# Performance work log

Hardware: AMD Instinct MI355X
Metric: run time of the kernel (lower is better)

The kernel has to match this reference:

```python
import jax, jax.numpy as jnp
import numpy as np

N_ENT = 100000
N_REL = 24
N_BASES = 8
HID = 256
N_EDGES = 1000000
N_TRIPLES = 65536


def _rgcn_layer(x, src, dst, edge_type, norm, basis, comp, root, bias):
    # x: [N, d]; basis: [B, d, d]; comp: [R, B]; root: [d, d]; bias: [d]
    x_src = x[src]                    # [E, d] gather
    coef = comp[edge_type]            # [E, B]
    out = x @ root + bias             # root/self transform
    # W_r = sum_b comp[r,b] * basis_b is linear, so aggregate coefficient- and
    # norm-weighted source features per basis, then apply basis once at node level.
    for b in range(basis.shape[0]):
        w = (coef[:, b] * norm)[:, None] * x_src          # [E, d]
        agg = jax.ops.segment_sum(w, dst, num_segments=N_ENT)  # [N, d]
        out = out + agg @ basis[b]
    return out


def _edge_norm(dst, edge_type):
    # PyG RGCNConv propagates per relation with aggr='mean': normalize by
    # in-degree of dst counted within each relation type.
    key = dst * N_REL + edge_type
    cnt = jax.ops.segment_sum(jnp.ones_like(key, dtype=jnp.float32), key,
                              num_segments=N_ENT * N_REL)
    return 1.0 / jnp.maximum(cnt[key], 1.0)


def setup_inputs() -> dict:
    key = jax.random.key(0)
    ks = jax.random.split(key, 16)
    d = HID
    xav_e = float(np.sqrt(6.0 / (N_ENT + d)))
    xav_r = float(np.sqrt(6.0 / (N_REL + d)))
    xav_w = float(np.sqrt(6.0 / (d + d)))
    inp = {
        'entity_emb': jax.random.uniform(ks[0], (N_ENT, d), jnp.float32, -xav_e, xav_e),
        'rel_emb': jax.random.uniform(ks[1], (N_REL, d), jnp.float32, -xav_r, xav_r),
        'basis1': jax.random.uniform(ks[2], (N_BASES, d, d), jnp.float32, -xav_w, xav_w),
        'comp1': jax.random.normal(ks[3], (N_REL, N_BASES), jnp.float32) / np.sqrt(N_BASES),
        'root1': jax.random.uniform(ks[4], (d, d), jnp.float32, -xav_w, xav_w),
        'bias1': jnp.zeros((d,), jnp.float32),
        'basis2': jax.random.uniform(ks[5], (N_BASES, d, d), jnp.float32, -xav_w, xav_w),
        'comp2': jax.random.normal(ks[6], (N_REL, N_BASES), jnp.float32) / np.sqrt(N_BASES),
        'root2': jax.random.uniform(ks[7], (d, d), jnp.float32, -xav_w, xav_w),
        'bias2': jnp.zeros((d,), jnp.float32),
        'edge_index': jax.random.randint(ks[8], (2, N_EDGES), 0, N_ENT, jnp.int32),
        'edge_type': jax.random.randint(ks[9], (N_EDGES,), 0, N_REL, jnp.int32),
        'heads': jax.random.randint(ks[10], (N_TRIPLES,), 0, N_ENT, jnp.int32),
        'rels': jax.random.randint(ks[11], (N_TRIPLES,), 0, N_REL, jnp.int32),
        'tails': jax.random.randint(ks[12], (N_TRIPLES,), 0, N_ENT, jnp.int32),
    }
    return inp


def reference(entity_emb, rel_emb, basis1, comp1, root1, bias1,
              basis2, comp2, root2, bias2,
              edge_index, edge_type, heads, rels, tails):
    src, dst = edge_index[0], edge_index[1]
    norm = _edge_norm(dst, edge_type)
    # eval mode: no edge dropout, feature dropout is identity
    x = entity_emb
    x = jax.nn.relu(_rgcn_layer(x, src, dst, edge_type, norm, basis1, comp1, root1, bias1))
    x = jax.nn.relu(_rgcn_layer(x, src, dst, edge_type, norm, basis2, comp2, root2, bias2))
    # DistMult score: sum(h * r * t)
    scores = jnp.sum(x[heads] * rel_emb[rels] * x[tails], axis=-1)
    return scores
```

## Files before the change

### kernel.cpp

```cpp
#include <hip/hip_runtime.h>
#include <hip/hip_bf16.h>

#define N_ENT   100000
#define N_REL   24
#define N_BASES 8
#define HID     256
#define N_EDGES 1000000
#define N_TRIPLES 65536

#define OFF_CNT    0ull
#define OFF_DEG    9600000ull
#define OFF_SMALL  10000000ull
#define OFF_SRCS   10004096ull
#define OFF_DSTS   14004096ull
#define OFF_NORMS  18004096ull
#define OFF_WHI    22004096ull
#define OFF_WLO    25149824ull
#define OFF_H1     28295552ull
#define OFF_H2     130695552ull
#define OFF_DRANK  233095552ull
#define OFF_ROWPTR 237095552ull
#define OFF_CUR2   237495680ull
#define OFF_BSUM   237895680ull
#define OFF_TMP    237897728ull
#define NEED_TOTAL 1261897728ull

typedef __attribute__((ext_vector_type(8))) short bf16x8;
typedef __attribute__((ext_vector_type(4))) float f32x4;

__device__ __forceinline__ void atomF(float* p, float v) {
#if defined(__HIP_PLATFORM_AMD__)
    unsafeAtomicAdd(p, v);
#else
    atomicAdd(p, v);
#endif
}
__device__ __forceinline__ void ntstore(float* p, float v) {
    __builtin_nontemporal_store(v, p);
}
__device__ __forceinline__ unsigned short f2bf(float f) {
    unsigned int u = __builtin_bit_cast(unsigned int, f);
    u += 0x7fffu + ((u >> 16) & 1u);
    return (unsigned short)(u >> 16);
}
__device__ __forceinline__ float bf2f(unsigned short h) {
    return __builtin_bit_cast(float, (unsigned int)h << 16);
}

__global__ __launch_bounds__(256) void count_kernel(
    const int* __restrict__ src, const int* __restrict__ dst,
    const int* __restrict__ et, int* __restrict__ cnt, int* __restrict__ hist,
    int* __restrict__ deg)
{
    __shared__ int lhist[N_REL];
    if (threadIdx.x < N_REL) lhist[threadIdx.x] = 0;
    __syncthreads();
    int stride = gridDim.x * blockDim.x;
    for (int e = blockIdx.x * blockDim.x + threadIdx.x; e < N_EDGES; e += stride) {
        int d = dst[e], t = et[e];
        atomicAdd(&cnt[d * N_REL + t], 1);
        atomicAdd(&deg[d], 1);
        atomicAdd(&lhist[t], 1);
    }
    __syncthreads();
    if (threadIdx.x < N_REL) atomicAdd(&hist[threadIdx.x], lhist[threadIdx.x]);
}

__global__ void prefix_kernel(const int* __restrict__ hist, int* offs,
                              int* cursor, int* tileoffs)
{
    if (threadIdx.x == 0) {
        int off = 0, toff = 0;
        for (int r = 0; r < N_REL; ++r) {
            offs[r] = off; cursor[r] = off; tileoffs[r] = toff;
            off  += hist[r];
            toff += (hist[r] + 63) >> 6;
        }
        offs[N_REL] = off; tileoffs[N_REL] = toff;
    }
}

#define SC_CHUNK 512
__global__ __launch_bounds__(256) void scatter_kernel(
    const int* __restrict__ src, const int* __restrict__ dst,
    const int* __restrict__ et, const int* __restrict__ cnt, int* cursor,
    int* __restrict__ srcS, int* __restrict__ dstS, float* __restrict__ normS)
{
    __shared__ int lhist[N_REL];
    __shared__ int lbase[N_REL];
    int tid = threadIdx.x;
    int base_e = blockIdx.x * SC_CHUNK;
    if (tid < N_REL) lhist[tid] = 0;
    __syncthreads();
    int myrank[2], myet[2];
    #pragma unroll
    for (int q = 0; q < 2; ++q) {
        int e = base_e + q * 256 + tid;
        if (e < N_EDGES) { myet[q] = et[e]; myrank[q] = atomicAdd(&lhist[myet[q]], 1); }
    }
    __syncthreads();
    if (tid < N_REL && lhist[tid] > 0) lbase[tid] = atomicAdd(&cursor[tid], lhist[tid]);
    __syncthreads();
    #pragma unroll
    for (int q = 0; q < 2; ++q) {
        int e = base_e + q * 256 + tid;
        if (e < N_EDGES) {
            int pos = lbase[myet[q]] + myrank[q];
            int d = dst[e];
            srcS[pos] = src[e];
            dstS[pos] = d;
            normS[pos] = 1.0f / (float)max(cnt[d * N_REL + myet[q]], 1);
        }
    }
}

#define SCAN_NB 391
__global__ __launch_bounds__(256) void scan_k1(
    const int* __restrict__ deg, int* __restrict__ rowptr, int* __restrict__ bsum)
{
    __shared__ int s[256];
    int i = threadIdx.x, b = blockIdx.x;
    int g = b * 256 + i;
    int v = (g < N_ENT) ? deg[g] : 0;
    s[i] = v;
    __syncthreads();
    for (int off = 1; off < 256; off <<= 1) {
        int t = (i >= off) ? s[i - off] : 0;
        __syncthreads();
        s[i] += t;
        __syncthreads();
    }
    if (g < N_ENT) rowptr[g] = s[i] - v;
    if (i == 255) bsum[b] = s[255];
}

__global__ __launch_bounds__(512) void scan_k2(int* __restrict__ bsum,
                                               int* __restrict__ rowptr)
{
    __shared__ int s[512];
    int i = threadIdx.x;
    int v = (i < SCAN_NB) ? bsum[i] : 0;
    s[i] = v;
    __syncthreads();
    for (int off = 1; off < 512; off <<= 1) {
        int t = (i >= off) ? s[i - off] : 0;
        __syncthreads();
        s[i] += t;
        __syncthreads();
    }
    if (i < SCAN_NB) bsum[i] = s[i] - v;
    if (i == SCAN_NB - 1) rowptr[N_ENT] = s[i];
}

__global__ __launch_bounds__(256) void scan_k3(
    int* __restrict__ rowptr, const int* __restrict__ bsum, int* __restrict__ cur2)
{
    int g = blockIdx.x * 256 + threadIdx.x;
    if (g < N_ENT) {
        int v = rowptr[g] + bsum[blockIdx.x];
        rowptr[g] = v;
        cur2[g] = v;
    }
}

__global__ __launch_bounds__(256) void drank_kernel(
    const int* __restrict__ dstS, int* __restrict__ cur2, int* __restrict__ drank)
{
    int p = blockIdx.x * 256 + threadIdx.x;
    if (p < N_EDGES) drank[p] = atomicAdd(&cur2[dstS[p]], 1);
}

__global__ __launch_bounds__(256) void makew_pk(
    const float* __restrict__ basis, const float* __restrict__ comp,
    unsigned short* __restrict__ Wh, unsigned short* __restrict__ Wl)
{
    int idx = blockIdx.x * 256 + threadIdx.x;
    if (idx >= N_REL * 8 * 4 * 256) return;
    int col = idx & 255;
    int q   = (idx >> 8) & 3;
    int kb  = (idx >> 10) & 7;
    int r   = idx >> 13;
    float cf[N_BASES];
    #pragma unroll
    for (int b = 0; b < N_BASES; ++b) cf[b] = comp[r * N_BASES + b];
    unsigned short hh[8] __attribute__((aligned(16)));
    unsigned short ll[8] __attribute__((aligned(16)));
    #pragma unroll
    for (int j = 0; j < 8; ++j) {
        int k = kb * 32 + q * 8 + j;
        float acc = 0.f;
        #pragma unroll
        for (int b = 0; b < N_BASES; ++b)
            acc += cf[b] * basis[(b << 16) + (k << 8) + col];
        unsigned short h = f2bf(acc);
        unsigned short l = f2bf(acc - bf2f(h));
        hh[j] = h; ll[j] = l;
    }
    size_t base = ((size_t)(r * 8 + kb) * 256 + col) * 32 + q * 8;
    *(uint4*)&Wh[base] = *(const uint4*)hh;
    *(uint4*)&Wl[base] = *(const uint4*)ll;
}

template <bool RELU_IN>
__global__ __launch_bounds__(256) void root_gemm(
    const float* __restrict__ x, const float* __restrict__ root,
    const float* __restrict__ bias, float* __restrict__ out)
{
    __shared__ float As[64][HID];
    int tid = threadIdx.x;
    int row0 = blockIdx.x * 64;
    for (int it = 0; it < 16; ++it) {
        int row = (it << 2) + (tid >> 6);
        int c4  = (tid & 63) << 2;
        int grow = row0 + row;
        float4 v = make_float4(0.f, 0.f, 0.f, 0.f);
        if (grow < N_ENT) v = *(const float4*)(x + (size_t)grow * HID + c4);
        if (RELU_IN) {
            v.x = fmaxf(v.x, 0.f); v.y = fmaxf(v.y, 0.f);
            v.z = fmaxf(v.z, 0.f); v.w = fmaxf(v.w, 0.f);
        }
        *(float4*)&As[row][c4] = v;
    }
    __syncthreads();
    int eg = tid >> 5, cg = tid & 31;
    const float* wp = root + (cg << 3);
    float acc[8][8] = {{0.f}};
    for (int k = 0; k < HID; k += 4) {
        float4 a4[8];
        #pragma unroll
        for (int i = 0; i < 8; ++i) a4[i] = *(const float4*)&As[(eg << 3) + i][k];
        #pragma unroll
        for (int kk = 0; kk < 4; ++kk) {
            float4 w0 = *(const float4*)(wp + (size_t)(k + kk) * HID);
            float4 w1 = *(const float4*)(wp + (size_t)(k + kk) * HID + 4);
            #pragma unroll
            for (int i = 0; i < 8; ++i) {
                float a = kk == 0 ? a4[i].x : kk == 1 ? a4[i].y : kk == 2 ? a4[i].z : a4[i].w;
                acc[i][0] += a * w0.x; acc[i][1] += a * w0.y;
                acc[i][2] += a * w0.z; acc[i][3] += a * w0.w;
                acc[i][4] += a * w1.x; acc[i][5] += a * w1.y;
                acc[i][6] += a * w1.z; acc[i][7] += a * w1.w;
            }
        }
    }
    float4 b0 = *(const float4*)(bias + (cg << 3));
    float4 b1 = *(const float4*)(bias + (cg << 3) + 4);
    #pragma unroll
    for (int i = 0; i < 8; ++i) {
        int grow = row0 + (eg << 3) + i;
        if (grow < N_ENT) {
            float4 o0 = make_float4(acc[i][0] + b0.x, acc[i][1] + b0.y,
                                    acc[i][2] + b0.z, acc[i][3] + b0.w);
            float4 o1 = make_float4(acc[i][4] + b1.x, acc[i][5] + b1.y,
                                    acc[i][6] + b1.z, acc[i][7] + b1.w);
            *(float4*)(out + (size_t)grow * HID + (cg << 3))     = o0;
            *(float4*)(out + (size_t)grow * HID + (cg << 3) + 4) = o1;
        }
    }
}

template <bool RELU_IN, int MODE>
__global__ __launch_bounds__(256, 4) void edge_gemm_mfma(
    const float* __restrict__ x,
    const unsigned short* __restrict__ Wh, const unsigned short* __restrict__ Wl,
    const int* __restrict__ srcS, const int* __restrict__ dstS,
    const float* __restrict__ normS, const int* __restrict__ offs,
    const int* __restrict__ tileoffs, float* __restrict__ outp,
    const int* __restrict__ drank)
{
    __shared__ unsigned short Ah[64 * 128];
    __shared__ unsigned short Al[64 * 128];
    int b = blockIdx.x;
    if (b >= tileoffs[N_REL]) return;
    int r = 0;
    while (tileoffs[r + 1] <= b) ++r;
    int e0 = offs[r] + ((b - tileoffs[r]) << 6);
    int e1 = min(offs[r + 1], e0 + 64);
    int ne = e1 - e0;

    int tid = threadIdx.x;
    int wv = tid >> 6;
    int lane = tid & 63;
    int lc = lane & 15, lq = lane >> 4;
    const unsigned short* WhR = Wh + ((size_t)r << 16);
    const unsigned short* WlR = Wl + ((size_t)r << 16);

    f32x4 acc[4][4];
    #pragma unroll
    for (int mi = 0; mi < 4; ++mi)
        #pragma unroll
        for (int ni = 0; ni < 4; ++ni) acc[mi][ni] = (f32x4)0.f;

    for (int h = 0; h < 2; ++h) {
        for (int it = 0; it < 8; ++it) {
            int row = (it << 3) + (tid >> 5);
            int cc  = (tid & 31) << 2;
            float4 v = make_float4(0.f, 0.f, 0.f, 0.f);
            float nrm = 0.f;
            if (row < ne) {
                int s = srcS[e0 + row];
                nrm = normS[e0 + row];
                v = *(const float4*)(x + (size_t)s * HID + (h << 7) + cc);
            }
            if (RELU_IN) {
                v.x = fmaxf(v.x, 0.f); v.y = fmaxf(v.y, 0.f);
                v.z = fmaxf(v.z, 0.f); v.w = fmaxf(v.w, 0.f);
            }
            v.x *= nrm; v.y *= nrm; v.z *= nrm; v.w *= nrm;
            unsigned short hh[4] __attribute__((aligned(8)));
            unsigned short ll[4] __attribute__((aligned(8)));
            float vv[4] = {v.x, v.y, v.z, v.w};
            #pragma unroll
            for (int j = 0; j < 4; ++j) {
                unsigned short hb = f2bf(vv[j]);
                hh[j] = hb;
                ll[j] = f2bf(vv[j] - bf2f(hb));
            }
            int byt = (cc << 1) ^ ((row & 7) << 4);
            int us  = (row << 7) + (byt >> 1);
            *(ushort4*)&Ah[us] = *(const ushort4*)hh;
            *(ushort4*)&Al[us] = *(const ushort4*)ll;
        }
        __syncthreads();

        for (int kb = 0; kb < 4; ++kb) {
            int kbf = (h << 2) + kb;
            bf16x8 ah[4], al[4], bh[4], bl[4];
            #pragma unroll
            for (int mi = 0; mi < 4; ++mi) {
                int row = mi * 16 + lc;
                int byt = ((kb << 6) + (lq << 4)) ^ ((row & 7) << 4);
                int us  = (row << 7) + (byt >> 1);
                ah[mi] = *(const bf16x8*)&Ah[us];
                al[mi] = *(const bf16x8*)&Al[us];
            }
            #pragma unroll
            for (int ni = 0; ni < 4; ++ni) {
                int col = (wv << 6) + ni * 16 + lc;
                size_t bidx = ((size_t)(kbf << 8) + col) * 32 + (lq << 3);
                bh[ni] = *(const bf16x8*)&WhR[bidx];
                bl[ni] = *(const bf16x8*)&WlR[bidx];
            }
            #pragma unroll
            for (int mi = 0; mi < 4; ++mi)
                #pragma unroll
                for (int ni = 0; ni < 4; ++ni) {
                    acc[mi][ni] = __builtin_amdgcn_mfma_f32_16x16x32_bf16(
                        ah[mi], bh[ni], acc[mi][ni], 0, 0, 0);
                    acc[mi][ni] = __builtin_amdgcn_mfma_f32_16x16x32_bf16(
                        ah[mi], bl[ni], acc[mi][ni], 0, 0, 0);
                    acc[mi][ni] = __builtin_amdgcn_mfma_f32_16x16x32_bf16(
                        al[mi], bh[ni], acc[mi][ni], 0, 0, 0);
                }
        }
        if (h == 0) __syncthreads();
    }

    #pragma unroll
    for (int mi = 0; mi < 4; ++mi) {
        #pragma unroll
        for (int rr = 0; rr < 4; ++rr) {
            int e = mi * 16 + (lq << 2) + rr;
            if (e < ne) {
                if (MODE == 0) {
                    int drow = dstS[e0 + e];
                    float* op = outp + (size_t)drow * HID + (wv << 6) + lc;
                    #pragma unroll
                    for (int ni = 0; ni < 4; ++ni)
                        atomF(op + ni * 16, acc[mi][ni][rr]);
                } else {
                    int pos = drank[e0 + e];
                    float* op = outp + ((size_t)pos << 8) + (wv << 6) + lc;
                    #pragma unroll
                    for (int ni = 0; ni < 4; ++ni)
                        ntstore(op + ni * 16, acc[mi][ni][rr]);
                }
            }
        }
    }
}

__global__ __launch_bounds__(256) void seg_reduce(
    const float* __restrict__ tmp, const int* __restrict__ rowptr,
    float* __restrict__ out)
{
    int d = blockIdx.x * 4 + (threadIdx.x >> 6);
    if (d >= N_ENT) return;
    int lane = threadIdx.x & 63;
    int j0 = rowptr[d], j1 = rowptr[d + 1];
    f32x4 acc = (f32x4)0.f;
    int j = j0;
    for (; j + 1 < j1; j += 2) {
        f32x4 v0 = __builtin_nontemporal_load(
            (const f32x4*)(tmp + ((size_t)j << 8) + (lane << 2)));
        f32x4 v1 = __builtin_nontemporal_load(
            (const f32x4*)(tmp + ((size_t)(j + 1) << 8) + (lane << 2)));
        acc += v0 + v1;
    }
    if (j < j1) {
        acc += __builtin_nontemporal_load(
            (const f32x4*)(tmp + ((size_t)j << 8) + (lane << 2)));
    }
    float* op = out + (size_t)d * HID + (lane << 2);
    f32x4 o = *(const f32x4*)op;
    o += acc;
    *(f32x4*)op = o;
}

__global__ __launch_bounds__(256) void distmult_kernel(
    const float* __restrict__ h2, const float* __restrict__ rel,
    const int* __restrict__ heads, const int* __restrict__ rels,
    const int* __restrict__ tails, float* __restrict__ scores)
{
    int tid = threadIdx.x;
    int tr = blockIdx.x * 4 + (tid >> 6);
    int lane = tid & 63;
    if (tr >= N_TRIPLES) return;
    int h = heads[tr], r = rels[tr], t = tails[tr];
    float4 a = *(const float4*)(h2 + (size_t)h * HID + lane * 4);
    float4 bb = *(const float4*)(rel + (size_t)r * HID + lane * 4);
    float4 c = *(const float4*)(h2 + (size_t)t * HID + lane * 4);
    a.x = fmaxf(a.x, 0.f); a.y = fmaxf(a.y, 0.f); a.z = fmaxf(a.z, 0.f); a.w = fmaxf(a.w, 0.f);
    c.x = fmaxf(c.x, 0.f); c.y = fmaxf(c.y, 0.f); c.z = fmaxf(c.z, 0.f); c.w = fmaxf(c.w, 0.f);
    float acc = a.x * bb.x * c.x + a.y * bb.y * c.y + a.z * bb.z * c.z + a.w * bb.w * c.w;
    #pragma unroll
    for (int off = 32; off >= 1; off >>= 1) acc += __shfl_xor(acc, off, 64);
    if (lane == 0) scores[tr] = acc;
}

extern "C" void kernel_launch(void* const* d_in, const int* in_sizes, int n_in,
                              void* d_out, int out_size, void* d_ws, size_t ws_size,
                              hipStream_t stream)
{
    const float* entity  = (const float*)d_in[0];
    const float* rel_emb = (const float*)d_in[1];
    const float* basis1  = (const float*)d_in[2];
    const float* comp1   = (const float*)d_in[3];
    const float* root1   = (const float*)d_in[4];
    const float* bias1   = (const float*)d_in[5];
    const float* basis2  = (const float*)d_in[6];
    const float* comp2   = (const float*)d_in[7];
    const float* root2   = (const float*)d_in[8];
    const float* bias2   = (const float*)d_in[9];
    const int* eidx  = (const int*)d_in[10];
    const int* etype = (const int*)d_in[11];
    const int* heads = (const int*)d_in[12];
    const int* rels  = (const int*)d_in[13];
    const int* tails = (const int*)d_in[14];
    const int* src = eidx;
    const int* dst = eidx + N_EDGES;

    char* ws = (char*)d_ws;
    int*   cnt      = (int*)(ws + OFF_CNT);
    int*   deg      = (int*)(ws + OFF_DEG);
    int*   small    = (int*)(ws + OFF_SMALL);
    int*   hist     = small;
    int*   offs     = small + 32;
    int*   cursor   = small + 64;
    int*   tileoffs = small + 96;
    int*   srcS   = (int*)(ws + OFF_SRCS);
    int*   dstS   = (int*)(ws + OFF_DSTS);
    float* normS  = (float*)(ws + OFF_NORMS);
    unsigned short* Whi = (unsigned short*)(ws + OFF_WHI);
    unsigned short* Wlo = (unsigned short*)(ws + OFF_WLO);
    float* h1     = (float*)(ws + OFF_H1);
    float* h2     = (float*)(ws + OFF_H2);
    int*   drank  = (int*)(ws + OFF_DRANK);
    int*   rowptr = (int*)(ws + OFF_ROWPTR);
    int*   cur2   = (int*)(ws + OFF_CUR2);
    int*   bsum   = (int*)(ws + OFF_BSUM);
    float* tmp    = (float*)(ws + OFF_TMP);

    const bool two_phase = (ws_size >= NEED_TOTAL);

    hipMemsetAsync(ws, 0, OFF_SMALL + 4096, stream);

    count_kernel<<<2048, 256, 0, stream>>>(src, dst, etype, cnt, hist, deg);
    prefix_kernel<<<1, 64, 0, stream>>>(hist, offs, cursor, tileoffs);
    scatter_kernel<<<(N_EDGES + SC_CHUNK - 1) / SC_CHUNK, 256, 0, stream>>>(
        src, dst, etype, cnt, cursor, srcS, dstS, normS);

    if (two_phase) {
        scan_k1<<<SCAN_NB, 256, 0, stream>>>(deg, rowptr, bsum);
        scan_k2<<<1, 512, 0, stream>>>(bsum, rowptr);
        scan_k3<<<SCAN_NB, 256, 0, stream>>>(rowptr, bsum, cur2);
        drank_kernel<<<(N_EDGES + 255) / 256, 256, 0, stream>>>(dstS, cur2, drank);
    }

    int egrid = N_EDGES / 64 + N_REL;
    int rgrid = (N_ENT + 63) / 64;
    int wgrid = (N_REL * 8 * 4 * 256 + 255) / 256;
    int sgrid = (N_ENT + 3) / 4;

    makew_pk<<<wgrid, 256, 0, stream>>>(basis1, comp1, Whi, Wlo);
    root_gemm<false><<<rgrid, 256, 0, stream>>>(entity, root1, bias1, h1);
    if (two_phase) {
        edge_gemm_mfma<false, 1><<<egrid, 256, 0, stream>>>(
            entity, Whi, Wlo, srcS, dstS, normS, offs, tileoffs, tmp, drank);
        seg_reduce<<<sgrid, 256, 0, stream>>>(tmp, rowptr, h1);
    } else {
        edge_gemm_mfma<false, 0><<<egrid, 256, 0, stream>>>(
            entity, Whi, Wlo, srcS, dstS, normS, offs, tileoffs, h1, drank);
    }

    makew_pk<<<wgrid, 256, 0, stream>>>(basis2, comp2, Whi, Wlo);
    root_gemm<true><<<rgrid, 256, 0, stream>>>(h1, root2, bias2, h2);
    if (two_phase) {
        edge_gemm_mfma<true, 1><<<egrid, 256, 0, stream>>>(
            h1, Whi, Wlo, srcS, dstS, normS, offs, tileoffs, tmp, drank);
        seg_reduce<<<sgrid, 256, 0, stream>>>(tmp, rowptr, h2);
    } else {
        edge_gemm_mfma<true, 0><<<egrid, 256, 0, stream>>>(
            h1, Whi, Wlo, srcS, dstS, normS, offs, tileoffs, h2, drank);
    }

    distmult_kernel<<<N_TRIPLES / 4, 256, 0, stream>>>(
        h2, rel_emb, heads, rels, tails, (float*)d_out);
}
```

Before: 2.974 ms.

## Aggregate per-basis node features before GEMM instead of per-edge relation GEMMs

```diff
diff --git a/kernel.cpp b/kernel.cpp
--- a/kernel.cpp
+++ b/kernel.cpp
@@ -7,6 +7,7 @@
 #define HID     256
 #define N_EDGES 1000000
 #define N_TRIPLES 65536
+#define CHUNK   25000
 
 #define OFF_CNT    0ull
 #define OFF_DEG    9600000ull
@@ -18,12 +19,16 @@
 #define OFF_WLO    25149824ull
 #define OFF_H1     28295552ull
 #define OFF_H2     130695552ull
-#define OFF_DRANK  233095552ull
-#define OFF_ROWPTR 237095552ull
-#define OFF_CUR2   237495680ull
-#define OFF_BSUM   237895680ull
-#define OFF_TMP    237897728ull
-#define NEED_TOTAL 1261897728ull
+#define OFF_ROWPTR 233095552ull
+#define OFF_CUR2   233495680ull
+#define OFF_BSUM   233895680ull
+#define OFF_SRCD   233897728ull
+#define OFF_ETD    237897728ull
+#define OFF_NORMD  241897728ull
+#define OFF_BPKH   245897728ull
+#define OFF_BPKL   246946304ull
+#define OFF_AGG    247994880ull
+#define NEED_NEW   452794880ull
 
 typedef __attribute__((ext_vector_type(8))) short bf16x8;
 typedef __attribute__((ext_vector_type(4))) float f32x4;
@@ -34,9 +39,6 @@
 #else
     atomicAdd(p, v);
 #endif
-}
-__device__ __forceinline__ void ntstore(float* p, float v) {
-    __builtin_nontemporal_store(v, p);
 }
 __device__ __forceinline__ unsigned short f2bf(float f) {
     unsigned int u = __builtin_bit_cast(unsigned int, f);
@@ -163,11 +165,42 @@
     }
 }
 
-__global__ __launch_bounds__(256) void drank_kernel(
-    const int* __restrict__ dstS, int* __restrict__ cur2, int* __restrict__ drank)
-{
-    int p = blockIdx.x * 256 + threadIdx.x;
-    if (p < N_EDGES) drank[p] = atomicAdd(&cur2[dstS[p]], 1);
+__global__ __launch_bounds__(256) void dstsort_kernel(
+    const int* __restrict__ src, const int* __restrict__ dst,
+    const int* __restrict__ et, const int* __restrict__ cnt, int* __restrict__ cur2,
+    int* __restrict__ srcD, int* __restrict__ etD, float* __restrict__ normD)
+{
+    int e = blockIdx.x * 256 + threadIdx.x;
+    if (e < N_EDGES) {
+        int d = dst[e], t = et[e];
+        int pos = atomicAdd(&cur2[d], 1);
+        srcD[pos] = src[e];
+        etD[pos] = t;
+        normD[pos] = 1.0f / (float)max(cnt[d * N_REL + t], 1);
+    }
+}
+
+__global__ __launch_bounds__(256) void bpack_kernel(
+    const float* __restrict__ basis, unsigned short* __restrict__ Bh,
+    unsigned short* __restrict__ Bl)
+{
+    int idx = blockIdx.x * 256 + threadIdx.x;
+    int col = idx & 255;
+    int q   = (idx >> 8) & 3;
+    int kb  = idx >> 10;
+    unsigned short hh[8] __attribute__((aligned(16)));
+    unsigned short ll[8] __attribute__((aligned(16)));
+    #pragma unroll
+    for (int j = 0; j < 8; ++j) {
+        int k = kb * 32 + q * 8 + j;
+        int b = k >> 8, kr = k & 255;
+        float a = basis[(b << 16) + (kr << 8) + col];
+        unsigned short h = f2bf(a);
+        hh[j] = h; ll[j] = f2bf(a - bf2f(h));
+    }
+    size_t base = ((size_t)kb * 256 + col) * 32 + q * 8;
+    *(uint4*)&Bh[base] = *(const uint4*)hh;
+    *(uint4*)&Bl[base] = *(const uint4*)ll;
 }
 
 __global__ __launch_bounds__(256) void makew_pk(
@@ -193,8 +226,7 @@
         for (int b = 0; b < N_BASES; ++b)
             acc += cf[b] * basis[(b << 16) + (k << 8) + col];
         unsigned short h = f2bf(acc);
-        unsigned short l = f2bf(acc - bf2f(h));
-        hh[j] = h; ll[j] = l;
+        hh[j] = h; ll[j] = f2bf(acc - bf2f(h));
     }
     size_t base = ((size_t)(r * 8 + kb) * 256 + col) * 32 + q * 8;
     *(uint4*)&Wh[base] = *(const uint4*)hh;
@@ -259,14 +291,140 @@
     }
 }
 
-template <bool RELU_IN, int MODE>
+template <bool RELU_IN>
+__global__ __launch_bounds__(256) void agg_kernel(
+    const float* __restrict__ x, const int* __restrict__ srcD,
+    const int* __restrict__ etD, const float* __restrict__ normD,
+    const int* __restrict__ rowptr, const float* __restrict__ comp,
+    float* __restrict__ agg, int c0)
+{
+    int d = c0 + blockIdx.x * 4 + (threadIdx.x >> 6);
+    if (d >= N_ENT) return;
+    int lane = threadIdx.x & 63;
+    f32x4 acc[N_BASES];
+    #pragma unroll
+    for (int b = 0; b < N_BASES; ++b) acc[b] = (f32x4)0.f;
+    int j1 = rowptr[d + 1];
+    for (int j = rowptr[d]; j < j1; ++j) {
+        int s = srcD[j];
+        float nm = normD[j];
+        int t = etD[j];
+        f32x4 v = *(const f32x4*)(x + (size_t)s * HID + (lane << 2));
+        if (RELU_IN) {
+            #pragma unroll
+            for (int q = 0; q < 4; ++q) v[q] = fmaxf(v[q], 0.f);
+        }
+        #pragma unroll
+        for (int b = 0; b < N_BASES; ++b)
+            acc[b] += v * (comp[t * N_BASES + b] * nm);
+    }
+    float* op = agg + ((size_t)(d - c0) << 11) + (lane << 2);
+    #pragma unroll
+    for (int b = 0; b < N_BASES; ++b)
+        __builtin_nontemporal_store(acc[b], (f32x4*)(op + (b << 8)));
+}
+
+__global__ __launch_bounds__(256, 4) void node_gemm(
+    const float* __restrict__ agg,
+    const unsigned short* __restrict__ Bh, const unsigned short* __restrict__ Bl,
+    float* __restrict__ hout, int c0)
+{
+    __shared__ unsigned short Ah[64 * 128];
+    __shared__ unsigned short Al[64 * 128];
+    int nrows = min(CHUNK, N_ENT - c0);
+    int m0 = blockIdx.x * 64;
+    if (m0 >= nrows) return;
+
+    int tid = threadIdx.x;
+    int wv = tid >> 6;
+    int lane = tid & 63;
+    int lc = lane & 15, lq = lane >> 4;
+
+    f32x4 acc[4][4];
+    #pragma unroll
+    for (int mi = 0; mi < 4; ++mi)
+        #pragma unroll
+        for (int ni = 0; ni < 4; ++ni) acc[mi][ni] = (f32x4)0.f;
+
+    for (int h = 0; h < 16; ++h) {
+        for (int it = 0; it < 8; ++it) {
+            int row = (it << 3) + (tid >> 5);
+            int cc  = (tid & 31) << 2;
+            f32x4 v = (f32x4)0.f;
+            if (m0 + row < nrows)
+                v = __builtin_nontemporal_load(
+                    (const f32x4*)(agg + ((size_t)(m0 + row) << 11) + (h << 7) + cc));
+            unsigned short hh[4] __attribute__((aligned(8)));
+            unsigned short ll[4] __attribute__((aligned(8)));
+            #pragma unroll
+            for (int j = 0; j < 4; ++j) {
+                unsigned short hb = f2bf(v[j]);
+                hh[j] = hb;
+                ll[j] = f2bf(v[j] - bf2f(hb));
+            }
+            int byt = (cc << 1) ^ ((row & 7) << 4);
+            int us  = (row << 7) + (byt >> 1);
+            *(ushort4*)&Ah[us] = *(const ushort4*)hh;
+            *(ushort4*)&Al[us] = *(const ushort4*)ll;
+        }
+        __syncthreads();
+
+        for (int kb = 0; kb < 4; ++kb) {
+            int kbf = (h << 2) + kb;
+            bf16x8 ah[4], al[4], bh[4], bl[4];
+            #pragma unroll
+            for (int mi = 0; mi < 4; ++mi) {
+                int row = mi * 16 + lc;
+                int byt = ((kb << 6) + (lq << 4)) ^ ((row & 7) << 4);
+                int us  = (row << 7) + (byt >> 1);
+                ah[mi] = *(const bf16x8*)&Ah[us];
+                al[mi] = *(const bf16x8*)&Al[us];
+            }
+            #pragma unroll
+            for (int ni = 0; ni < 4; ++ni) {
+                int col = (wv << 6) + ni * 16 + lc;
+                size_t bidx = ((size_t)(kbf << 8) + col) * 32 + (lq << 3);
+                bh[ni] = *(const bf16x8*)&Bh[bidx];
+                bl[ni] = *(const bf16x8*)&Bl[bidx];
+            }
+            #pragma unroll
+            for (int mi = 0; mi < 4; ++mi)
+                #pragma unroll
+                for (int ni = 0; ni < 4; ++ni) {
+                    acc[mi][ni] = __builtin_amdgcn_mfma_f32_16x16x32_bf16(
+                        ah[mi], bh[ni], acc[mi][ni], 0, 0, 0);
+                    acc[mi][ni] = __builtin_amdgcn_mfma_f32_16x16x32_bf16(
+                        ah[mi], bl[ni], acc[mi][ni], 0, 0, 0);
+                    acc[mi][ni] = __builtin_amdgcn_mfma_f32_16x16x32_bf16(
+                        al[mi], bh[ni], acc[mi][ni], 0, 0, 0);
+                }
+        }
+        if (h < 15) __syncthreads();
+    }
+
+    #pragma unroll
+    for (int mi = 0; mi < 4; ++mi) {
+        #pragma unroll
+        for (int rr = 0; rr < 4; ++rr) {
+            int e = mi * 16 + (lq << 2) + rr;
+            if (m0 + e < nrows) {
+                int grow = c0 + m0 + e;
+                float* op = hout + (size_t)grow * HID + (wv << 6) + lc;
+                #pragma unroll
+                for (int ni = 0; ni < 4; ++ni)
+                    op[ni * 16] += acc[mi][ni][rr];
+            }
+        }
+    }
+}
+
+template <bool RELU_IN>
 __global__ __launch_bounds__(256, 4) void edge_gemm_mfma(
     const float* __restrict__ x,
     const unsigned short* __restrict__ Wh, const unsigned short* __restrict__ Wl,
     const int* __restrict__ srcS, const int* __restrict__ dstS,
     const float* __restrict__ normS, const int* __restrict__ offs,
-    const int* __restrict__ tileoffs, float* __restrict__ outp,
-    const int* __restrict__ drank)
+    const int* __restrict__ tileoffs, float* __restrict__ outp)
 {
     __shared__ unsigned short Ah[64 * 128];
     __shared__ unsigned short Al[64 * 128];
@@ -362,49 +520,14 @@
         for (int rr = 0; rr < 4; ++rr) {
             int e = mi * 16 + (lq << 2) + rr;
             if (e < ne) {
-                if (MODE == 0) {
-                    int drow = dstS[e0 + e];
-                    float* op = outp + (size_t)drow * HID + (wv << 6) + lc;
-                    #pragma unroll
-                    for (int ni = 0; ni < 4; ++ni)
-                        atomF(op + ni * 16, acc[mi][ni][rr]);
-                } else {
-                    int pos = drank[e0 + e];
-                    float* op = outp + ((size_t)pos << 8) + (wv << 6) + lc;
-                    #pragma unroll
-                    for (int ni = 0; ni < 4; ++ni)
-                        ntstore(op + ni * 16, acc[mi][ni][rr]);
-                }
-            }
-        }
-    }
-}
-
-__global__ __launch_bounds__(256) void seg_reduce(
-    const float* __restrict__ tmp, const int* __restrict__ rowptr,
-    float* __restrict__ out)
-{
-    int d = blockIdx.x * 4 + (threadIdx.x >> 6);
-    if (d >= N_ENT) return;
-    int lane = threadIdx.x & 63;
-    int j0 = rowptr[d], j1 = rowptr[d + 1];
-    f32x4 acc = (f32x4)0.f;
-    int j = j0;
-    for (; j + 1 < j1; j += 2) {
-        f32x4 v0 = __builtin_nontemporal_load(
-            (const f32x4*)(tmp + ((size_t)j << 8) + (lane << 2)));
-        f32x4 v1 = __builtin_nontemporal_load(
-            (const f32x4*)(tmp + ((size_t)(j + 1) << 8) + (lane << 2)));
-        acc += v0 + v1;
-    }
-    if (j < j1) {
-        acc += __builtin_nontemporal_load(
-            (const f32x4*)(tmp + ((size_t)j << 8) + (lane << 2)));
-    }
-    float* op = out + (size_t)d * HID + (lane << 2);
-    f32x4 o = *(const f32x4*)op;
-    o += acc;
-    *(f32x4*)op = o;
+                int drow = dstS[e0 + e];
+                float* op = outp + (size_t)drow * HID + (wv << 6) + lc;
+                #pragma unroll
+                for (int ni = 0; ni < 4; ++ni)
+                    atomF(op + ni * 16, acc[mi][ni][rr]);
+            }
+        }
+    }
 }
 
 __global__ __launch_bounds__(256) void distmult_kernel(
@@ -465,53 +588,65 @@
     unsigned short* Wlo = (unsigned short*)(ws + OFF_WLO);
     float* h1     = (float*)(ws + OFF_H1);
     float* h2     = (float*)(ws + OFF_H2);
-    int*   drank  = (int*)(ws + OFF_DRANK);
     int*   rowptr = (int*)(ws + OFF_ROWPTR);
     int*   cur2   = (int*)(ws + OFF_CUR2);
     int*   bsum   = (int*)(ws + OFF_BSUM);
-    float* tmp    = (float*)(ws + OFF_TMP);
-
-    const bool two_phase = (ws_size >= NEED_TOTAL);
+    int*   srcD   = (int*)(ws + OFF_SRCD);
+    int*   etD    = (int*)(ws + OFF_ETD);
+    float* normD  = (float*)(ws + OFF_NORMD);
+    unsigned short* Bh = (unsigned short*)(ws + OFF_BPKH);
+    unsigned short* Bl = (unsigned short*)(ws + OFF_BPKL);
+    float* agg    = (float*)(ws + OFF_AGG);
+
+    const bool newpath = (ws_size >= NEED_NEW);
 
     hipMemsetAsync(ws, 0, OFF_SMALL + 4096, stream);
 
     count_kernel<<<2048, 256, 0, stream>>>(src, dst, etype, cnt, hist, deg);
-    prefix_kernel<<<1, 64, 0, stream>>>(hist, offs, cursor, tileoffs);
-    scatter_kernel<<<(N_EDGES + SC_CHUNK - 1) / SC_CHUNK, 256, 0, stream>>>(
-        src, dst, etype, cnt, cursor, srcS, dstS, normS);
-
-    if (two_phase) {
+
+    int rgrid = (N_ENT + 63) / 64;
+
+    if (newpath) {
         scan_k1<<<SCAN_NB, 256, 0, stream>>>(deg, rowptr, bsum);
         scan_k2<<<1, 512, 0, stream>>>(bsum, rowptr);
         scan_k3<<<SCAN_NB, 256, 0, stream>>>(rowptr, bsum, cur2);
-        drank_kernel<<<(N_EDGES + 255) / 256, 256, 0, stream>>>(dstS, cur2, drank);
-    }
-
-    int egrid = N_EDGES / 64 + N_REL;
-    int rgrid = (N_ENT + 63) / 64;
-    int wgrid = (N_REL * 8 * 4 * 256 + 255) / 256;
-    int sgrid = (N_ENT + 3) / 4;
-
-    makew_pk<<<wgrid, 256, 0, stream>>>(basis1, comp1, Whi, Wlo);
-    root_gemm<false><<<rgrid, 256, 0, stream>>>(entity, root1, bias1, h1);
-    if (two_phase) {
-        edge_gemm_mfma<false, 1><<<egrid, 256, 0, stream>>>(
-            entity, Whi, Wlo, srcS, dstS, normS, offs, tileoffs, tmp, drank);
-        seg_reduce<<<sgrid, 256, 0, stream>>>(tmp, rowptr, h1);
+        dstsort_kernel<<<(N_EDGES + 255) / 256, 256, 0, stream>>>(
+            src, dst, etype, cnt, cur2, srcD, etD, normD);
+
+        int ggrid = (CHUNK + 63) / 64;
+        int agrid = CHUNK / 4;
+
+        bpack_kernel<<<256, 256, 0, stream>>>(basis1, Bh, Bl);
+        root_gemm<false><<<rgrid, 256, 0, stream>>>(entity, root1, bias1, h1);
+        for (int c = 0; c < N_ENT / CHUNK; ++c) {
+            agg_kernel<false><<<agrid, 256, 0, stream>>>(
+                entity, srcD, etD, normD, rowptr, comp1, agg, c * CHUNK);
+            node_gemm<<<ggrid, 256, 0, stream>>>(agg, Bh, Bl, h1, c * CHUNK);
+        }
+
+        bpack_kernel<<<256, 256, 0, stream>>>(basis2, Bh, Bl);
+        root_gemm<true><<<rgrid, 256, 0, stream>>>(h1, root2, bias2, h2);
+        for (int c = 0; c < N_ENT / CHUNK; ++c) {
+            agg_kernel<true><<<agrid, 256, 0, stream>>>(
+                h1, srcD, etD, normD, rowptr, comp2, agg, c * CHUNK);
+            node_gemm<<<ggrid, 256, 0, stream>>>(agg, Bh, Bl, h2, c * CHUNK);
+        }
     } else {
-        edge_gemm_mfma<false, 0><<<egrid, 256, 0, stream>>>(
-            entity, Whi, Wlo, srcS, dstS, normS, offs, tileoffs, h1, drank);
-    }
-
-    makew_pk<<<wgrid, 256, 0, stream>>>(basis2, comp2, Whi, Wlo);
-    root_gemm<true><<<rgrid, 256, 0, stream>>>(h1, root2, bias2, h2);
-    if (two_phase) {
-        edge_gemm_mfma<true, 1><<<egrid, 256, 0, stream>>>(
-            h1, Whi, Wlo, srcS, dstS, normS, offs, tileoffs, tmp, drank);
-        seg_reduce<<<sgrid, 256, 0, stream>>>(tmp, rowptr, h2);
-    } else {
-        edge_gemm_mfma<true, 0><<<egrid, 256, 0, stream>>>(
-            h1, Whi, Wlo, srcS, dstS, normS, offs, tileoffs, h2, drank);
+        prefix_kernel<<<1, 64, 0, stream>>>(hist, offs, cursor, tileoffs);
+        scatter_kernel<<<(N_EDGES + SC_CHUNK - 1) / SC_CHUNK, 256, 0, stream>>>(
+            src, dst, etype, cnt, cursor, srcS, dstS, normS);
+        int egrid = N_EDGES / 64 + N_REL;
+        int wgrid = (N_REL * 8 * 4 * 256 + 255) / 256;
+
+        makew_pk<<<wgrid, 256, 0, stream>>>(basis1, comp1, Whi, Wlo);
+        root_gemm<false><<<rgrid, 256, 0, stream>>>(entity, root1, bias1, h1);
+        edge_gemm_mfma<false><<<egrid, 256, 0, stream>>>(
+            entity, Whi, Wlo, srcS, dstS, normS, offs, tileoffs, h1);
+
+        makew_pk<<<wgrid, 256, 0, stream>>>(basis2, comp2, Whi, Wlo);
+        root_gemm<true><<<rgrid, 256, 0, stream>>>(h1, root2, bias2, h2);
+        edge_gemm_mfma<true><<<egrid, 256, 0, stream>>>(
+            h1, Whi, Wlo, srcS, dstS, normS, offs, tileoffs, h2);
     }
 
     distmult_kernel<<<N_TRIPLES / 4, 256, 0, stream>>>(
```

Measured after the change: 2.974 ms. Within noise of the previous version (-0.0%).
